# Kernel optimization log

Measured on AMD Instinct MI355X. Metric: run time of the kernel, lower is better.

The kernel has to match this reference:

```python
import jax, jax.numpy as jnp
import numpy as np

B, M, D, H = 2, 2048, 1024, 16


def _rope(x):
    # Equivalent to x.transpose(0,1) @ R[:m] with R the block-diagonal 2x2
    # rotation matrices from get_rotary_matrix (note the (i-1) in theta,
    # faithful to the source).
    b, m, d = x.shape
    i = jnp.arange(d // 2, dtype=jnp.float32)
    theta = 10000.0 ** (-2.0 * (i - 1.0) / d)           # [d/2]
    ang = jnp.arange(m, dtype=jnp.float32)[:, None] * theta[None, :]  # [m, d/2]
    c, s = jnp.cos(ang), jnp.sin(ang)
    xe, xo = x[..., 0::2], x[..., 1::2]                 # [b, m, d/2]
    ye = xe * c + xo * s                                # out[2i]   = q[2i]*cos + q[2i+1]*sin
    yo = -xe * s + xo * c                               # out[2i+1] = -q[2i]*sin + q[2i+1]*cos
    return jnp.stack([ye, yo], axis=-1).reshape(b, m, d)


def setup_inputs() -> dict:
    key = jax.random.key(0)
    ks = jax.random.split(key, 8)
    w = lambda k, shape: (jax.random.normal(k, shape, jnp.float32) * 0.02)
    return {
        "x": jax.random.normal(ks[0], (B, M, D), jnp.float32),
        "wq": w(ks[1], (D, D)),
        "wk": w(ks[2], (D, D)),
        "wv": w(ks[3], (D, D)),
        "in_proj_w": w(ks[4], (3 * D, D)),
        "in_proj_b": w(ks[5], (3 * D,)),
        "out_w": w(ks[6], (D, D)),
        "out_b": w(ks[7], (D,)),
    }


def reference(x, wq, wk, wv, in_proj_w, in_proj_b, out_w, out_b):
    b, m, d = x.shape
    h = H
    hd = d // h
    # bias-free QKV projections, each followed by the dense RoPE rotation
    q = _rope(x @ wq.T)
    k = _rope(x @ wk.T)
    v = _rope(x @ wv.T)
    # nn.MultiheadAttention: packed in_proj, scaled dot-product, causal mask, out_proj
    wqi, wki, wvi = jnp.split(in_proj_w, 3, axis=0)
    bqi, bki, bvi = jnp.split(in_proj_b, 3, axis=0)
    qh = (q @ wqi.T + bqi).reshape(b, m, h, hd)
    kh = (k @ wki.T + bki).reshape(b, m, h, hd)
    vh = (v @ wvi.T + bvi).reshape(b, m, h, hd)
    scores = jnp.einsum("bqhd,bkhd->bhqk", qh, kh) / jnp.sqrt(jnp.float32(hd))
    causal = jnp.tril(jnp.ones((m, m), dtype=bool))
    scores = jnp.where(causal, scores, jnp.float32(-jnp.inf))
    attn = jax.nn.softmax(scores, axis=-1)              # dropout p=0.0
    o = jnp.einsum("bhqk,bkhd->bqhd", attn, vh).reshape(b, m, d)
    return o @ out_w.T + out_b
```

## Files before the change

### kernel.cpp

```cpp
#include <hip/hip_runtime.h>
#include <hip/hip_bf16.h>
#include <math.h>

typedef __bf16 bf16;
typedef __bf16 bf16x4 __attribute__((ext_vector_type(4)));
typedef __bf16 bf16x8 __attribute__((ext_vector_type(8)));
typedef float  f32x4  __attribute__((ext_vector_type(4)));

#define MM 2048
#define DD 1024
#define HD 64

__device__ __forceinline__ void gload16(const void* g, void* l) {
  __builtin_amdgcn_global_load_lds((const __attribute__((address_space(1))) void*)g,
                                   (__attribute__((address_space(3))) void*)l, 16, 0, 0);
}

__global__ __launch_bounds__(256) void k_cvt_all(
    const float* __restrict__ x,   const float* __restrict__ wq,
    const float* __restrict__ wk,  const float* __restrict__ wv,
    const float* __restrict__ ipw, const float* __restrict__ ow,
    bf16* __restrict__ xb,  bf16* __restrict__ wqb, bf16* __restrict__ wkb,
    bf16* __restrict__ wvb, bf16* __restrict__ ipwb, bf16* __restrict__ owb)
{
  int bid = blockIdx.x;
  const float* s; bf16* d; int base;
  if (bid < 4096)       { s = x;   d = xb;   base = bid; }
  else if (bid < 5120)  { s = wq;  d = wqb;  base = bid - 4096; }
  else if (bid < 6144)  { s = wk;  d = wkb;  base = bid - 5120; }
  else if (bid < 7168)  { s = wv;  d = wvb;  base = bid - 6144; }
  else if (bid < 10240) { s = ipw; d = ipwb; base = bid - 7168; }
  else                  { s = ow;  d = owb;  base = bid - 10240; }
  int i = base*256 + threadIdx.x;
  float4 v = ((const float4*)s)[i];
  bf16x4 o;
  o[0]=(bf16)v.x; o[1]=(bf16)v.y; o[2]=(bf16)v.z; o[3]=(bf16)v.w;
  ((bf16x4*)d)[i] = o;
}

__device__ __forceinline__ void gemm_core8(const bf16* __restrict__ A,
                                           const bf16* __restrict__ Bw,
                                           const int row0, const int col0,
                                           bf16* __restrict__ sA, bf16* __restrict__ sB,
                                           f32x4 (&acc)[2][4])
{
  const int t = threadIdx.x;
  #pragma unroll
  for (int m=0;m<2;m++)
    #pragma unroll
    for (int n=0;n<4;n++)
      acc[m][n] = (f32x4){0.f,0.f,0.f,0.f};

  const int srow = t >> 3;
  const int lch  = ((t & 7) - (srow & 7)) & 7;
  const bf16* gA = A  + (size_t)(row0 + srow)*DD + lch*8;
  const bf16* gB = Bw + (size_t)(col0 + srow)*DD + lch*8;
  char* lA = (char*)sA + t*16;
  char* lB = (char*)sB + t*16;

  const int lane = t & 63, wid = t >> 6;
  const int wr = wid >> 1, wc = wid & 1;
  const int fr = lane & 15, fg = lane >> 4;
  const int fr7 = fr & 7;

  gload16(gA,                 lA);
  gload16(gA + (size_t)64*DD, lA + 8192);
  gload16(gB,                 lB);
  gload16(gB + (size_t)64*DD, lB + 8192);

  for (int kt = 0; kt < 16; ++kt) {
    const int buf = kt & 1;
    __builtin_amdgcn_s_barrier();
    if (kt < 15) {
      const int nb = buf ^ 1;
      const int ko = (kt + 1) * 64;
      gload16(gA + ko,                 lA + nb*16384);
      gload16(gA + (size_t)64*DD + ko, lA + nb*16384 + 8192);
      gload16(gB + ko,                 lB + nb*16384);
      gload16(gB + (size_t)64*DD + ko, lB + nb*16384 + 8192);
      asm volatile("s_waitcnt vmcnt(4)" ::: "memory");
    } else {
      asm volatile("s_waitcnt vmcnt(0)" ::: "memory");
    }
    __builtin_amdgcn_s_barrier();
    const char* bA = (const char*)sA + buf*16384;
    const char* bB = (const char*)sB + buf*16384;
    bf16x8 aF[2][2], bF[2][4];
    #pragma unroll
    for (int kb=0;kb<2;kb++) {
      #pragma unroll
      for (int m=0;m<2;m++)
        aF[kb][m] = *(const bf16x8*)(bA + (wr*32 + m*16 + fr)*128 + ((kb*4 + fg + fr7)&7)*16);
      #pragma unroll
      for (int n=0;n<4;n++)
        bF[kb][n] = *(const bf16x8*)(bB + (wc*64 + n*16 + fr)*128 + ((kb*4 + fg + fr7)&7)*16);
    }
    __builtin_amdgcn_s_setprio(1);
    #pragma unroll
    for (int kb=0;kb<2;kb++)
      #pragma unroll
      for (int m=0;m<2;m++)
        #pragma unroll
        for (int n=0;n<4;n++)
          acc[m][n] = __builtin_amdgcn_mfma_f32_16x16x32_bf16(aF[kb][m], bF[kb][n], acc[m][n], 0, 0, 0);
    __builtin_amdgcn_s_setprio(0);
  }
}

__global__ __launch_bounds__(512, 2) void k_gemm_rope(
    const bf16* __restrict__ X, const bf16* __restrict__ Wq,
    const bf16* __restrict__ Wk, const bf16* __restrict__ Wv,
    bf16* __restrict__ QKV)
{
  __shared__ bf16 sA[2*128*64];
  __shared__ bf16 sB[2*128*64];
  const int row0 = blockIdx.x * 128;
  const int col0 = blockIdx.y * 128;
  const int z = blockIdx.z;
  const bf16* Bw = (z==0) ? Wq : ((z==1) ? Wk : Wv);
  f32x4 acc[2][4];
  gemm_core8(X, Bw, row0, col0, sA, sB, acc);

  bf16* outp = QKV + (size_t)z * (4096u*1024u);
  const int lane = threadIdx.x & 63, wid = threadIdx.x >> 6;
  const int wr = wid >> 1, wc = wid & 1;
  const int fr = lane & 15, fg = lane >> 4;
  #pragma unroll
  for (int n=0;n<4;n++) {
    const int gc = col0 + wc*64 + n*16 + fr;
    const int i2 = gc >> 1;
    const float theta = __expf(((float)i2 - 1.0f) * (-2.0f * 9.210340371976184f / 1024.0f));
    #pragma unroll
    for (int m=0;m<2;m++) {
      #pragma unroll
      for (int r=0;r<4;r++) {
        const int gr = row0 + wr*32 + m*16 + fg*4 + r;
        const float v  = acc[m][n][r];
        const float pv = __shfl_xor(v, 1);
        const int pos = gr & (MM-1);
        float sv, cv;
        __sincosf((float)pos * theta, &sv, &cv);
        const float res = (gc & 1) ? (v*cv - pv*sv) : (v*cv + pv*sv);
        outp[(size_t)gr * DD + gc] = (bf16)res;
      }
    }
  }
}

__global__ __launch_bounds__(512, 2) void k_gemm_proj(
    const bf16* __restrict__ QKV, const bf16* __restrict__ IPW,
    const float* __restrict__ IPB,
    bf16* __restrict__ QH, bf16* __restrict__ KH, bf16* __restrict__ VT)
{
  __shared__ bf16 sA[2*128*64];
  __shared__ bf16 sB[2*128*64];
  const int row0 = blockIdx.x * 128;
  const int col0 = blockIdx.y * 128;
  const int z = blockIdx.z;
  const bf16* A  = QKV + (size_t)z * (4096u*1024u);
  const bf16* Bw = IPW + (size_t)z * (1024u*1024u);
  const float* bias = IPB + z * DD;
  f32x4 acc[2][4];
  gemm_core8(A, Bw, row0, col0, sA, sB, acc);

  const int lane = threadIdx.x & 63, wid = threadIdx.x >> 6;
  const int wr = wid >> 1, wc = wid & 1;
  const int fr = lane & 15, fg = lane >> 4;
  if (z < 2) {
    bf16* outp = (z==0) ? QH : KH;
    const float vscale = (z==0) ? 0.18033688011112042f : 1.0f;
    #pragma unroll
    for (int n=0;n<4;n++) {
      const int gc = col0 + wc*64 + n*16 + fr;
      const float bs = bias[gc];
      #pragma unroll
      for (int m=0;m<2;m++) {
        #pragma unroll
        for (int r=0;r<4;r++) {
          const int gr = row0 + wr*32 + m*16 + fg*4 + r;
          outp[(size_t)gr * DD + gc] = (bf16)((acc[m][n][r] + bs) * vscale);
        }
      }
    }
  } else {
    #pragma unroll
    for (int n=0;n<4;n++) {
      const int gc = col0 + wc*64 + n*16 + fr;
      const float bs = bias[gc];
      #pragma unroll
      for (int m=0;m<2;m++) {
        const int gr0 = row0 + wr*32 + m*16 + fg*4;
        const int b  = gr0 >> 11;
        const int m0 = gr0 & (MM-1);
        bf16x4 pk;
        #pragma unroll
        for (int r=0;r<4;r++) pk[r] = (bf16)(acc[m][n][r] + bs);
        *(bf16x4*)(VT + ((size_t)b*DD + gc)*MM + m0) = pk;
      }
    }
  }
}

__global__ __launch_bounds__(256) void k_attn(
    const bf16* __restrict__ QH, const bf16* __restrict__ KH,
    const bf16* __restrict__ VT, bf16* __restrict__ O)
{
  __shared__ bf16 sK[2*64*64];
  __shared__ bf16 sV[2*64*64];
  __shared__ bf16 sP[4*16*64];
  const int idx = blockIdx.x;
  const int xcd = idx & 7;
  const int rr  = idx >> 3;
  const int combo = xcd*4 + (rr & 3);
  const int b = combo >> 4, h = combo & 15;
  const int qt = 31 - (rr >> 2);
  const int t = threadIdx.x, lane = t & 63, wid = t >> 6;
  const int fr = lane & 15, fg = lane >> 4;
  const int swzP = (fr & 7) << 4;
  const int q0 = qt * 64;
  const int qg = q0 + wid*16 + fr;

  const int srow = t >> 3;
  const int cc   = (t & 7) ^ (srow & 7);
  const bf16* gK0 = KH + ((size_t)b*MM + srow)*DD + h*HD + cc*8;
  const bf16* gK1 = gK0 + (size_t)32*DD;
  const bf16* gV0 = VT + ((size_t)b*DD + h*HD + srow)*MM + cc*8;
  const bf16* gV1 = gV0 + (size_t)32*MM;
  char* lK = (char*)sK + t*16;
  char* lV = (char*)sV + t*16;
  char* sPw = (char*)(sP + wid*16*64);

  const bf16* qp = QH + ((size_t)b*MM + qg)*DD + h*HD + fg*8;
  bf16x8 aQ0 = *(const bf16x8*)qp;
  bf16x8 aQ1 = *(const bf16x8*)(qp + 32);

  bf16x8 ones;
  #pragma unroll
  for (int j=0;j<8;j++) ones[j] = (bf16)1.0f;

  gload16(gK0, lK);  gload16(gK1, lK + 4096);
  gload16(gV0, lV);  gload16(gV1, lV + 4096);

  f32x4 o_acc[4];
  #pragma unroll
  for (int n=0;n<4;n++) o_acc[n] = (f32x4){0.f,0.f,0.f,0.f};
  f32x4 lacc = (f32x4){0.f,0.f,0.f,0.f};

  for (int kt = 0; kt <= qt; ++kt) {
    const int buf = kt & 1;
    asm volatile("s_waitcnt vmcnt(0)" ::: "memory");
    __builtin_amdgcn_s_barrier();
    if (kt < qt) {
      const int nb = buf ^ 1;
      gload16(gK0 + (size_t)(kt+1)*64*DD, lK + nb*8192);
      gload16(gK1 + (size_t)(kt+1)*64*DD, lK + nb*8192 + 4096);
      gload16(gV0 + (kt+1)*64,            lV + nb*8192);
      gload16(gV1 + (kt+1)*64,            lV + nb*8192 + 4096);
    }
    const char* bKb = (const char*)sK + buf*8192;
    const char* bVb = (const char*)sV + buf*8192;

    f32x4 sacc[4];
    #pragma unroll
    for (int n=0;n<4;n++) sacc[n] = (f32x4){0.f,0.f,0.f,0.f};
    __builtin_amdgcn_s_setprio(1);
    #pragma unroll
    for (int kb=0;kb<2;kb++) {
      const bf16x8 q = kb ? aQ1 : aQ0;
      #pragma unroll
      for (int n=0;n<4;n++) {
        const int rowA = n*16 + fr;
        bf16x8 aK = *(const bf16x8*)(bKb + rowA*128 + ((kb*64 + fg*16) ^ ((rowA&7)<<4)));
        sacc[n] = __builtin_amdgcn_mfma_f32_16x16x32_bf16(aK, q, sacc[n], 0, 0, 0);
      }
    }
    __builtin_amdgcn_s_setprio(0);

    const bool diag = (kt == qt);
    float ps[16];
    #pragma unroll
    for (int n=0;n<4;n++)
      #pragma unroll
      for (int r=0;r<4;r++) {
        float xx = sacc[n][r] - 32.0f;
        if (diag) {
          const int kvg = kt*64 + n*16 + fg*4 + r;
          if (kvg > qg) xx = -INFINITY;
        }
        ps[n*4+r] = exp2f(xx);
      }
    #pragma unroll
    for (int n=0;n<4;n++) {
      bf16x4 pk;
      #pragma unroll
      for (int r=0;r<4;r++) pk[r] = (bf16)ps[n*4+r];
      *(bf16x4*)(sPw + fr*128 + ((n*32 + fg*8) ^ swzP)) = pk;
    }
    asm volatile("s_waitcnt lgkmcnt(0)" ::: "memory");

    bf16x8 aP0 = *(const bf16x8*)(sPw + fr*128 + ((fg*16) ^ swzP));
    bf16x8 aP1 = *(const bf16x8*)(sPw + fr*128 + ((64 + fg*16) ^ swzP));
    __builtin_amdgcn_s_setprio(1);
    #pragma unroll
    for (int n=0;n<4;n++) {
      const int rowV = n*16 + fr;
      bf16x8 bV0 = *(const bf16x8*)(bVb + rowV*128 + ((fg*16) ^ ((rowV&7)<<4)));
      bf16x8 bV1 = *(const bf16x8*)(bVb + rowV*128 + ((64 + fg*16) ^ ((rowV&7)<<4)));
      o_acc[n] = __builtin_amdgcn_mfma_f32_16x16x32_bf16(aP0, bV0, o_acc[n], 0, 0, 0);
      o_acc[n] = __builtin_amdgcn_mfma_f32_16x16x32_bf16(aP1, bV1, o_acc[n], 0, 0, 0);
    }
    lacc = __builtin_amdgcn_mfma_f32_16x16x32_bf16(aP0, ones, lacc, 0, 0, 0);
    lacc = __builtin_amdgcn_mfma_f32_16x16x32_bf16(aP1, ones, lacc, 0, 0, 0);
    __builtin_amdgcn_s_setprio(0);
  }

  #pragma unroll
  for (int r=0;r<4;r++) {
    const int qq = q0 + wid*16 + fg*4 + r;
    const float inv = 1.0f / lacc[r];
    #pragma unroll
    for (int n=0;n<4;n++) {
      O[((size_t)b*MM + qq)*DD + h*HD + n*16 + fr] = (bf16)(o_acc[n][r] * inv);
    }
  }
}

__global__ __launch_bounds__(512, 2) void k_gemm_out(
    const bf16* __restrict__ A, const bf16* __restrict__ OW,
    const float* __restrict__ OBIAS, float* __restrict__ outp)
{
  __shared__ bf16 sA[2*128*64];
  __shared__ bf16 sB[2*128*64];
  const int row0 = blockIdx.x * 128;
  const int col0 = blockIdx.y * 128;
  f32x4 acc[2][4];
  gemm_core8(A, OW, row0, col0, sA, sB, acc);
  const int lane = threadIdx.x & 63, wid = threadIdx.x >> 6;
  const int wr = wid >> 1, wc = wid & 1;
  const int fr = lane & 15, fg = lane >> 4;
  #pragma unroll
  for (int n=0;n<4;n++) {
    const int gc = col0 + wc*64 + n*16 + fr;
    const float bs = OBIAS[gc];
    #pragma unroll
    for (int m=0;m<2;m++) {
      #pragma unroll
      for (int r=0;r<4;r++) {
        const int gr = row0 + wr*32 + m*16 + fg*4 + r;
        outp[(size_t)gr * DD + gc] = acc[m][n][r] + bs;
      }
    }
  }
}

extern "C" void kernel_launch(void* const* d_in, const int* in_sizes, int n_in,
                              void* d_out, int out_size, void* d_ws, size_t ws_size,
                              hipStream_t stream)
{
  (void)in_sizes; (void)n_in; (void)out_size; (void)ws_size;
  const float* x   = (const float*)d_in[0];
  const float* wq  = (const float*)d_in[1];
  const float* wk  = (const float*)d_in[2];
  const float* wv  = (const float*)d_in[3];
  const float* ipw = (const float*)d_in[4];
  const float* ipb = (const float*)d_in[5];
  const float* ow  = (const float*)d_in[6];
  const float* ob  = (const float*)d_in[7];
  float* outp = (float*)d_out;

  char* ws = (char*)d_ws;
  const size_t MB = 1u << 20;
  bf16* xb   = (bf16*)(ws + 0*MB);
  bf16* wqb  = (bf16*)(ws + 8*MB);
  bf16* wkb  = (bf16*)(ws + 10*MB);
  bf16* wvb  = (bf16*)(ws + 12*MB);
  bf16* ipwb = (bf16*)(ws + 14*MB);
  bf16* owb  = (bf16*)(ws + 20*MB);
  bf16* QKV  = (bf16*)(ws + 22*MB);
  bf16* QH   = (bf16*)(ws + 46*MB);
  bf16* KH   = (bf16*)(ws + 54*MB);
  bf16* VT   = (bf16*)(ws + 62*MB);
  bf16* Ob   = (bf16*)(ws + 70*MB);

  k_cvt_all<<<11264, 256, 0, stream>>>(x, wq, wk, wv, ipw, ow,
                                       xb, wqb, wkb, wvb, ipwb, owb);
  k_gemm_rope<<<dim3(32,8,3), 512, 0, stream>>>(xb, wqb, wkb, wvb, QKV);
  k_gemm_proj<<<dim3(32,8,3), 512, 0, stream>>>(QKV, ipwb, ipb, QH, KH, VT);
  k_attn<<<1024, 256, 0, stream>>>(QH, KH, VT, Ob);
  k_gemm_out<<<dim3(32,8,1), 512, 0, stream>>>(Ob, owb, ob, outp);
}
```

Measured before the change: 130.6 us.

## Enlarge attention query tile to 128 rows with 8 waves sharing K/V tiles

Each attention workgroup now covers 128 query rows with 512 threads (8 waves) instead of 64 rows with 4 waves, halving the grid. Each K/V tile loaded into LDS is reused by twice as many query rows, and each thread issues one async load per tile instead of two. Waves whose rows lie entirely before a key tile skip that tile, and the constant -32 offset is folded into the accumulator initialisation. The trade-off is fewer workgroups for load balancing, uneven work across waves on the diagonal tiles, and a barrier each iteration even for waves that skip the tile.

```diff
diff --git a/kernel.cpp b/kernel.cpp
--- a/kernel.cpp
+++ b/kernel.cpp
@@ -201,31 +201,30 @@
   }
 }
 
-__global__ __launch_bounds__(256) void k_attn(
+__global__ __launch_bounds__(512) void k_attn(
     const bf16* __restrict__ QH, const bf16* __restrict__ KH,
     const bf16* __restrict__ VT, bf16* __restrict__ O)
 {
   __shared__ bf16 sK[2*64*64];
   __shared__ bf16 sV[2*64*64];
-  __shared__ bf16 sP[4*16*64];
+  __shared__ bf16 sP[8*16*64];
   const int idx = blockIdx.x;
   const int xcd = idx & 7;
   const int rr  = idx >> 3;
   const int combo = xcd*4 + (rr & 3);
   const int b = combo >> 4, h = combo & 15;
-  const int qt = 31 - (rr >> 2);
+  const int qb = 15 - (rr >> 2);
   const int t = threadIdx.x, lane = t & 63, wid = t >> 6;
   const int fr = lane & 15, fg = lane >> 4;
   const int swzP = (fr & 7) << 4;
-  const int q0 = qt * 64;
+  const int q0 = qb * 128;
   const int qg = q0 + wid*16 + fr;
+  const int ntiles = 2*qb + 2;
 
   const int srow = t >> 3;
   const int cc   = (t & 7) ^ (srow & 7);
-  const bf16* gK0 = KH + ((size_t)b*MM + srow)*DD + h*HD + cc*8;
-  const bf16* gK1 = gK0 + (size_t)32*DD;
-  const bf16* gV0 = VT + ((size_t)b*DD + h*HD + srow)*MM + cc*8;
-  const bf16* gV1 = gV0 + (size_t)32*MM;
+  const bf16* gK = KH + ((size_t)b*MM + srow)*DD + h*HD + cc*8;
+  const bf16* gV = VT + ((size_t)b*DD + h*HD + srow)*MM + cc*8;
   char* lK = (char*)sK + t*16;
   char* lV = (char*)sV + t*16;
   char* sPw = (char*)(sP + wid*16*64);
@@ -238,31 +237,32 @@
   #pragma unroll
   for (int j=0;j<8;j++) ones[j] = (bf16)1.0f;
 
-  gload16(gK0, lK);  gload16(gK1, lK + 4096);
-  gload16(gV0, lV);  gload16(gV1, lV + 4096);
+  gload16(gK, lK);
+  gload16(gV, lV);
 
   f32x4 o_acc[4];
   #pragma unroll
   for (int n=0;n<4;n++) o_acc[n] = (f32x4){0.f,0.f,0.f,0.f};
   f32x4 lacc = (f32x4){0.f,0.f,0.f,0.f};
-
-  for (int kt = 0; kt <= qt; ++kt) {
+  const f32x4 minit = (f32x4){-32.f,-32.f,-32.f,-32.f};
+
+  for (int kt = 0; kt < ntiles; ++kt) {
     const int buf = kt & 1;
     asm volatile("s_waitcnt vmcnt(0)" ::: "memory");
     __builtin_amdgcn_s_barrier();
-    if (kt < qt) {
+    if (kt + 1 < ntiles) {
       const int nb = buf ^ 1;
-      gload16(gK0 + (size_t)(kt+1)*64*DD, lK + nb*8192);
-      gload16(gK1 + (size_t)(kt+1)*64*DD, lK + nb*8192 + 4096);
-      gload16(gV0 + (kt+1)*64,            lV + nb*8192);
-      gload16(gV1 + (kt+1)*64,            lV + nb*8192 + 4096);
-    }
+      gload16(gK + (size_t)(kt+1)*64*DD, lK + nb*8192);
+      gload16(gV + (kt+1)*64,            lV + nb*8192);
+    }
+    if (kt*64 > q0 + wid*16 + 15) continue;
+
     const char* bKb = (const char*)sK + buf*8192;
     const char* bVb = (const char*)sV + buf*8192;
 
     f32x4 sacc[4];
     #pragma unroll
-    for (int n=0;n<4;n++) sacc[n] = (f32x4){0.f,0.f,0.f,0.f};
+    for (int n=0;n<4;n++) sacc[n] = minit;
     __builtin_amdgcn_s_setprio(1);
     #pragma unroll
     for (int kb=0;kb<2;kb++) {
@@ -276,14 +276,14 @@
     }
     __builtin_amdgcn_s_setprio(0);
 
-    const bool diag = (kt == qt);
+    const bool needMask = (kt*64 + 63) > (q0 + wid*16);
     float ps[16];
     #pragma unroll
     for (int n=0;n<4;n++)
       #pragma unroll
       for (int r=0;r<4;r++) {
-        float xx = sacc[n][r] - 32.0f;
-        if (diag) {
+        float xx = sacc[n][r];
+        if (needMask) {
           const int kvg = kt*64 + n*16 + fg*4 + r;
           if (kvg > qg) xx = -INFINITY;
         }
@@ -386,6 +386,6 @@
                                        xb, wqb, wkb, wvb, ipwb, owb);
   k_gemm_rope<<<dim3(32,8,3), 512, 0, stream>>>(xb, wqb, wkb, wvb, QKV);
   k_gemm_proj<<<dim3(32,8,3), 512, 0, stream>>>(QKV, ipwb, ipb, QH, KH, VT);
-  k_attn<<<1024, 256, 0, stream>>>(QH, KH, VT, Ob);
+  k_attn<<<512, 512, 0, stream>>>(QH, KH, VT, Ob);
   k_gemm_out<<<dim3(32,8,1), 512, 0, stream>>>(Ob, owb, ob, outp);
 }
```

Result: slower. 141.4 us (+8.2%).
